# Optimization experiments

Hardware: AMD Instinct MI355X
Metric: run time of the kernel (lower is better)

## Reference

```python
import jax, jax.numpy as jnp
import numpy as np

NUM_CLASSES = 1000
FEAT_DIM = 256
MOMENTUM = 0.999
WARMUP_STEPS = 200


def setup_inputs() -> dict:
    key = jax.random.key(0)
    k1, k2, k3, k4, k5 = jax.random.split(key, 5)
    N, B, K = 200000, 64, 100
    features = jax.random.normal(k1, (N, FEAT_DIM), jnp.float32)
    labels = jax.random.randint(k2, (N,), 0, NUM_CLASSES)
    labels_per_image = jax.random.randint(k3, (B, K), 0, NUM_CLASSES)
    prototypes = jax.random.normal(k4, (NUM_CLASSES, FEAT_DIM), jnp.float32)
    init_mask = jax.random.randint(k5, (NUM_CLASSES,), 0, 2).astype(jnp.int32)
    cooccurrence = jnp.zeros((NUM_CLASSES, NUM_CLASSES), jnp.float32)
    return dict(features=features, labels=labels, labels_per_image=labels_per_image,
                prototypes=prototypes, init_mask=init_mask, cooccurrence=cooccurrence,
                step=5000)


def reference(features, labels, labels_per_image, prototypes, init_mask, cooccurrence, step):
    C = prototypes.shape[0]
    progress = min(1.0, float(step) / max(1, WARMUP_STEPS * 10))
    m = 0.99 + (MOMENTUM - 0.99) * progress

    # F.normalize(features, dim=-1) with eps=1e-12
    fn = features / jnp.clip(jnp.linalg.norm(features, axis=-1, keepdims=True), 1e-12)

    # per-class scatter-mean (replaces Python loop over labels.unique())
    counts = jax.ops.segment_sum(jnp.ones(labels.shape, jnp.float32), labels, num_segments=C)  # [C]
    sums = jax.ops.segment_sum(fn, labels, num_segments=C)                                      # [C, D]
    mean = sums / jnp.maximum(counts, 1.0)[:, None]

    present = (counts > 0)[:, None]          # class appears in this batch
    inited = (init_mask > 0)[:, None]        # prototype already initialized
    ema = m * prototypes + (1.0 - m) * mean
    new_protos = jnp.where(present & inited, ema, jnp.where(present & ~inited, mean, prototypes))
    new_init = ((init_mask > 0) | (counts > 0)).astype(jnp.int32)

    # co-occurrence: presence matrix P[B,C]; pair (ci,cj) gets +1 each direction per image
    B, K = labels_per_image.shape
    rows = jnp.repeat(jnp.arange(B), K)
    P = jnp.zeros((B, C), jnp.float32).at[rows, labels_per_image.reshape(-1)].set(1.0)
    cooc_add = (P.T @ P) * (1.0 - jnp.eye(C, dtype=jnp.float32))
    new_cooc = cooccurrence + cooc_add

    return new_protos, new_init, new_cooc
```

## Files before the change

kernel.cpp:

```cpp
#include <hip/hip_runtime.h>
#include <hip/hip_bf16.h>

#define NC 1000
#define FD 256
#define KPI 100
#define CAP 1024

__global__ void k_scatter(const int* __restrict__ labels, int n,
                          const int* __restrict__ lpi, int bk,
                          int* __restrict__ cursor,
                          unsigned long long* __restrict__ M,
                          int* __restrict__ rowidx) {
    int i = blockIdx.x * blockDim.x + threadIdx.x;
    if (i < n) {
        int lab = labels[i];
        int pos = atomicAdd(&cursor[lab], 1);
        if (pos < CAP) rowidx[lab * CAP + pos] = i;
    }
    if (i < bk) atomicOr(&M[lpi[i]], 1ull << (i / KPI));
}

__global__ __launch_bounds__(1024, 8) void k_proto(
    const float* __restrict__ feat, const int* __restrict__ rowidx,
    const int* __restrict__ cursor,
    const float* __restrict__ protos, const int* __restrict__ init_mask,
    const int* __restrict__ step,
    const unsigned long long* __restrict__ M,
    const float* __restrict__ cooc_in,
    float* __restrict__ out_protos, float* __restrict__ out_init,
    float* __restrict__ out_cooc) {
    int c = blockIdx.x;
    int tid = threadIdx.x;
    int lane = tid & 63;
    int w = tid >> 6;
    int cnt = cursor[c];
    if (cnt > CAP) cnt = CAP;
    int start = c * CAP;
    int end = start + cnt;

    const float4* f4 = (const float4*)feat;
    float ax = 0.f, ay = 0.f, az = 0.f, aw = 0.f;

    for (int base = start + 4 * w; base < end; base += 64) {
        int r[4];
        float4 v[4];
        float s[4];
        #pragma unroll
        for (int k = 0; k < 4; k++) {
            int idx = (base + k < end) ? (base + k) : (end - 1);
            r[k] = rowidx[idx];
        }
        #pragma unroll
        for (int k = 0; k < 4; k++) v[k] = f4[(size_t)r[k] * 64 + lane];
        #pragma unroll
        for (int k = 0; k < 4; k++)
            s[k] = v[k].x * v[k].x + v[k].y * v[k].y + v[k].z * v[k].z + v[k].w * v[k].w;
        #pragma unroll
        for (int o = 32; o; o >>= 1) {
            #pragma unroll
            for (int k = 0; k < 4; k++) s[k] += __shfl_xor(s[k], o);
        }
        #pragma unroll
        for (int k = 0; k < 4; k++) {
            float sc = (base + k < end) ? (1.0f / fmaxf(sqrtf(s[k]), 1e-12f)) : 0.0f;
            ax += v[k].x * sc;
            ay += v[k].y * sc;
            az += v[k].z * sc;
            aw += v[k].w * sc;
        }
    }

    __shared__ float4 sh4[1024];
    sh4[w * 64 + lane] = make_float4(ax, ay, az, aw);
    __syncthreads();

    if (tid < FD) {
        const float* shf = (const float*)sh4;
        int d = tid;
        float t = 0.f;
        #pragma unroll
        for (int q = 0; q < 16; q++) t += shf[q * 256 + d];
        float mean = t / fmaxf((float)cnt, 1.0f);

        float p = protos[c * FD + d];
        bool present = cnt > 0;
        bool inited = init_mask[c] > 0;
        float prog = fminf(1.0f, (float)step[0] / 2000.0f);
        float m = 0.99f + (0.999f - 0.99f) * prog;
        float ema = m * p + (1.0f - m) * mean;
        float outv = present ? (inited ? ema : mean) : p;
        out_protos[c * FD + d] = outv;
        if (tid == 0) out_init[c] = (inited || present) ? 1.0f : 0.0f;
    }

    if (tid < NC) {
        unsigned long long mi = M[c];
        float add = (c == tid) ? 0.0f : (float)__popcll(mi & M[tid]);
        out_cooc[c * NC + tid] = cooc_in[c * NC + tid] + add;
    }
}

extern "C" void kernel_launch(void* const* d_in, const int* in_sizes, int n_in,
                              void* d_out, int out_size, void* d_ws, size_t ws_size,
                              hipStream_t stream) {
    const float* feat      = (const float*)d_in[0];
    const int*   labels    = (const int*)d_in[1];
    const int*   lpi       = (const int*)d_in[2];
    const float* protos    = (const float*)d_in[3];
    const int*   init_mask = (const int*)d_in[4];
    const float* cooc      = (const float*)d_in[5];
    const int*   step      = (const int*)d_in[6];

    int n  = in_sizes[1];
    int bk = in_sizes[2];

    float* out_protos = (float*)d_out;
    float* out_init   = out_protos + (size_t)NC * FD;
    float* out_cooc   = out_init + NC;

    char* ws = (char*)d_ws;
    int* cursor           = (int*)(ws);
    unsigned long long* M = (unsigned long long*)(ws + 4096);
    int* rowidx           = (int*)(ws + 12288);

    hipMemsetAsync(d_ws, 0, 12288, stream);

    int big = n > bk ? n : bk;
    k_scatter<<<(big + 255) / 256, 256, 0, stream>>>(labels, n, lpi, bk, cursor, M, rowidx);
    k_proto<<<NC, 1024, 0, stream>>>(feat, rowidx, cursor, protos, init_mask, step,
                                     M, cooc, out_protos, out_init, out_cooc);
}
```

Baseline: 344.0 us.

## Normalize features in streaming pass and scatter fp16 rows into class buckets

The first kernel now reads features contiguously, L2-normalizes each row with a wavefront reduction, and writes the normalized row as fp16 into a per-class bucket slot. The finalize kernel then sums contiguous fp16 bucket rows instead of gathering fp32 rows through an index list. The goal is to replace random row gathers with a coalesced stream plus a half-size scatter. In exchange every feature is written once more, accumulation uses fp16-rounded values, and the per-class cap drops to 512, which could truncate classes holding more than 512 rows.

```diff
diff --git a/kernel.cpp b/kernel.cpp
--- a/kernel.cpp
+++ b/kernel.cpp
@@ -1,28 +1,67 @@
 #include <hip/hip_runtime.h>
-#include <hip/hip_bf16.h>
+#include <hip/hip_fp16.h>
 
 #define NC 1000
 #define FD 256
 #define KPI 100
-#define CAP 1024
+#define CAP 512
 
-__global__ void k_scatter(const int* __restrict__ labels, int n,
-                          const int* __restrict__ lpi, int bk,
-                          int* __restrict__ cursor,
-                          unsigned long long* __restrict__ M,
-                          int* __restrict__ rowidx) {
-    int i = blockIdx.x * blockDim.x + threadIdx.x;
-    if (i < n) {
-        int lab = labels[i];
-        int pos = atomicAdd(&cursor[lab], 1);
-        if (pos < CAP) rowidx[lab * CAP + pos] = i;
+union H4 { __half2 h[2]; uint2 u; };
+
+__global__ __launch_bounds__(256) void k_norm_scatter(
+    const float* __restrict__ feat, const int* __restrict__ labels, int n,
+    const int* __restrict__ lpi, int bk,
+    int* __restrict__ cursor, unsigned long long* __restrict__ M,
+    uint2* __restrict__ buckets) {
+    int tid = threadIdx.x;
+    int lane = tid & 63;
+    int w = tid >> 6;
+    int gw = blockIdx.x * 4 + w;
+    int gid = blockIdx.x * 256 + tid;
+    int nw = gridDim.x * 4;
+
+    if (gid < bk) atomicOr(&M[lpi[gid]], 1ull << (gid / KPI));
+
+    const float4* f4 = (const float4*)feat;
+    for (int r0 = gw * 2; r0 < n; r0 += nw * 2) {
+        int r1 = r0 + 1;
+        bool ok1 = r1 < n;
+        float4 a = f4[(size_t)r0 * 64 + lane];
+        float4 b = f4[(size_t)(ok1 ? r1 : r0) * 64 + lane];
+        float s0 = a.x * a.x + a.y * a.y + a.z * a.z + a.w * a.w;
+        float s1 = b.x * b.x + b.y * b.y + b.z * b.z + b.w * b.w;
+        #pragma unroll
+        for (int o = 32; o; o >>= 1) {
+            s0 += __shfl_xor(s0, o);
+            s1 += __shfl_xor(s1, o);
+        }
+        float sc0 = 1.0f / fmaxf(sqrtf(s0), 1e-12f);
+        float sc1 = 1.0f / fmaxf(sqrtf(s1), 1e-12f);
+
+        int lab0 = 0, lab1 = 0, pos0 = 0, pos1 = 0;
+        if (lane == 0) {
+            lab0 = labels[r0];
+            pos0 = atomicAdd(&cursor[lab0], 1);
+            if (ok1) {
+                lab1 = labels[r1];
+                pos1 = atomicAdd(&cursor[lab1], 1);
+            }
+        }
+        lab0 = __shfl(lab0, 0); pos0 = __shfl(pos0, 0);
+        lab1 = __shfl(lab1, 0); pos1 = __shfl(pos1, 0);
+
+        H4 p0, p1;
+        p0.h[0] = __floats2half2_rn(a.x * sc0, a.y * sc0);
+        p0.h[1] = __floats2half2_rn(a.z * sc0, a.w * sc0);
+        p1.h[0] = __floats2half2_rn(b.x * sc1, b.y * sc1);
+        p1.h[1] = __floats2half2_rn(b.z * sc1, b.w * sc1);
+        if (pos0 < CAP) buckets[((size_t)lab0 * CAP + pos0) * 64 + lane] = p0.u;
+        if (ok1 && pos1 < CAP) buckets[((size_t)lab1 * CAP + pos1) * 64 + lane] = p1.u;
     }
-    if (i < bk) atomicOr(&M[lpi[i]], 1ull << (i / KPI));
 }
 
-__global__ __launch_bounds__(1024, 8) void k_proto(
-    const float* __restrict__ feat, const int* __restrict__ rowidx,
-    const int* __restrict__ cursor,
+__global__ __launch_bounds__(1024, 8) void k_finalize(
+    const uint2* __restrict__ buckets, const int* __restrict__ cursor,
     const float* __restrict__ protos, const int* __restrict__ init_mask,
     const int* __restrict__ step,
     const unsigned long long* __restrict__ M,
@@ -34,39 +73,24 @@
     int lane = tid & 63;
     int w = tid >> 6;
     int cnt = cursor[c];
-    if (cnt > CAP) cnt = CAP;
-    int start = c * CAP;
-    int end = start + cnt;
+    int cntd = cnt > CAP ? CAP : cnt;
 
-    const float4* f4 = (const float4*)feat;
+    const uint2* base = buckets + (size_t)c * CAP * 64;
     float ax = 0.f, ay = 0.f, az = 0.f, aw = 0.f;
 
-    for (int base = start + 4 * w; base < end; base += 64) {
-        int r[4];
-        float4 v[4];
-        float s[4];
-        #pragma unroll
-        for (int k = 0; k < 4; k++) {
-            int idx = (base + k < end) ? (base + k) : (end - 1);
-            r[k] = rowidx[idx];
-        }
-        #pragma unroll
-        for (int k = 0; k < 4; k++) v[k] = f4[(size_t)r[k] * 64 + lane];
-        #pragma unroll
-        for (int k = 0; k < 4; k++)
-            s[k] = v[k].x * v[k].x + v[k].y * v[k].y + v[k].z * v[k].z + v[k].w * v[k].w;
-        #pragma unroll
-        for (int o = 32; o; o >>= 1) {
-            #pragma unroll
-            for (int k = 0; k < 4; k++) s[k] += __shfl_xor(s[k], o);
-        }
-        #pragma unroll
-        for (int k = 0; k < 4; k++) {
-            float sc = (base + k < end) ? (1.0f / fmaxf(sqrtf(s[k]), 1e-12f)) : 0.0f;
-            ax += v[k].x * sc;
-            ay += v[k].y * sc;
-            az += v[k].z * sc;
-            aw += v[k].w * sc;
+    for (int r = w; r < cntd; r += 32) {
+        int r2 = r + 16;
+        bool ok2 = r2 < cntd;
+        uint2 q0 = base[(size_t)r * 64 + lane];
+        uint2 q1 = base[(size_t)(ok2 ? r2 : r) * 64 + lane];
+        H4 h0, h1; h0.u = q0; h1.u = q1;
+        float2 f00 = __half22float2(h0.h[0]);
+        float2 f01 = __half22float2(h0.h[1]);
+        ax += f00.x; ay += f00.y; az += f01.x; aw += f01.y;
+        if (ok2) {
+            float2 f10 = __half22float2(h1.h[0]);
+            float2 f11 = __half22float2(h1.h[1]);
+            ax += f10.x; ay += f10.y; az += f11.x; aw += f11.y;
         }
     }
 
@@ -74,22 +98,28 @@
     sh4[w * 64 + lane] = make_float4(ax, ay, az, aw);
     __syncthreads();
 
-    if (tid < FD) {
-        const float* shf = (const float*)sh4;
-        int d = tid;
-        float t = 0.f;
+    if (tid < 64) {
+        float4 s = make_float4(0.f, 0.f, 0.f, 0.f);
         #pragma unroll
-        for (int q = 0; q < 16; q++) t += shf[q * 256 + d];
-        float mean = t / fmaxf((float)cnt, 1.0f);
-
-        float p = protos[c * FD + d];
+        for (int q = 0; q < 16; q++) {
+            float4 t = sh4[q * 64 + tid];
+            s.x += t.x; s.y += t.y; s.z += t.z; s.w += t.w;
+        }
+        float inv = 1.0f / fmaxf((float)cnt, 1.0f);
         bool present = cnt > 0;
         bool inited = init_mask[c] > 0;
         float prog = fminf(1.0f, (float)step[0] / 2000.0f);
         float m = 0.99f + (0.999f - 0.99f) * prog;
-        float ema = m * p + (1.0f - m) * mean;
-        float outv = present ? (inited ? ema : mean) : p;
-        out_protos[c * FD + d] = outv;
+
+        const float4* p4 = (const float4*)(protos + (size_t)c * FD);
+        float4 p = p4[tid];
+        float4 o;
+        #define EMA1(mc, pc) (present ? (inited ? (m * (pc) + (1.0f - m) * ((mc) * inv)) \
+                                                : ((mc) * inv)) : (pc))
+        o.x = EMA1(s.x, p.x); o.y = EMA1(s.y, p.y);
+        o.z = EMA1(s.z, p.z); o.w = EMA1(s.w, p.w);
+        #undef EMA1
+        ((float4*)(out_protos + (size_t)c * FD))[tid] = o;
         if (tid == 0) out_init[c] = (inited || present) ? 1.0f : 0.0f;
     }
 
@@ -121,12 +151,12 @@
     char* ws = (char*)d_ws;
     int* cursor           = (int*)(ws);
     unsigned long long* M = (unsigned long long*)(ws + 4096);
-    int* rowidx           = (int*)(ws + 12288);
+    uint2* buckets        = (uint2*)(ws + 16384);
 
     hipMemsetAsync(d_ws, 0, 12288, stream);
 
-    int big = n > bk ? n : bk;
-    k_scatter<<<(big + 255) / 256, 256, 0, stream>>>(labels, n, lpi, bk, cursor, M, rowidx);
-    k_proto<<<NC, 1024, 0, stream>>>(feat, rowidx, cursor, protos, init_mask, step,
-                                     M, cooc, out_protos, out_init, out_cooc);
+    k_norm_scatter<<<2048, 256, 0, stream>>>(feat, labels, n, lpi, bk,
+                                             cursor, M, buckets);
+    k_finalize<<<NC, 1024, 0, stream>>>(buckets, cursor, protos, init_mask, step,
+                                        M, cooc, out_protos, out_init, out_cooc);
 }
```

Measured after the change: 340.5 us. No clear change (-1.0%).
